# Kernel optimization log

Measured on AMD Instinct MI355X. Metric: run time of the kernel, lower is better.

The kernel has to match this reference:

```python
import jax, jax.numpy as jnp
import numpy as np

N, D, H, O, E = 50000, 512, 512, 256, 150000
NEG_SLOPE = 0.2
EPS = 1e-16


def gat_conv(x, edge_index, W_src, W_dst, a_src, a_dst, bias):
    """Single-head PyG GATConv, add_self_loops=False.
    x: [N, Din]; edge_index: [2, E] (row 0 = src, row 1 = dst).
    W_src/W_dst: [Din, C]; a_src/a_dst: [C]; bias: [C].
    """
    src, dst = edge_index[0], edge_index[1]
    h_src = x @ W_src                      # [N, C]
    h_dst = x @ W_dst                      # [N, C]
    alpha_src = h_src @ a_src              # [N]
    alpha_dst = h_dst @ a_dst              # [N]
    e = jax.nn.leaky_relu(alpha_src[src] + alpha_dst[dst], NEG_SLOPE)  # [E]
    # per-destination segment softmax (numerically stable)
    m = jax.ops.segment_max(e, dst, num_segments=N)       # [N]
    ex = jnp.exp(e - m[dst])                               # [E]
    s = jax.ops.segment_sum(ex, dst, num_segments=N)       # [N]
    alpha = ex / (s[dst] + EPS)                            # [E]
    # scatter-add weighted source messages to destinations
    out = jax.ops.segment_sum(alpha[:, None] * h_src[src], dst, num_segments=N)  # [N, C]
    return out + bias


def setup_inputs() -> dict:
    key = jax.random.key(0)
    ks = jax.random.split(key, 20)
    g = lambda i, shape, sc: (jax.random.normal(ks[i], shape, dtype=jnp.float32) * sc)
    inp = {
        "x": jax.random.normal(ks[0], (N, D), dtype=jnp.float32),
        "edge_index": jax.random.randint(ks[1], (2, E), 0, N, dtype=jnp.int32),
        "edge_index_2_hop": jax.random.randint(ks[2], (2, E), 0, N, dtype=jnp.int32),
        # conv1 (D -> H)
        "W1_src": g(3, (D, H), 0.05), "W1_dst": g(4, (D, H), 0.05),
        "a1_src": g(5, (H,), 0.05), "a1_dst": g(6, (H,), 0.05),
        "b1": jnp.zeros((H,), jnp.float32),
        # lin1 (H -> H)
        "Wl1": g(7, (H, H), 0.05), "bl1": jnp.zeros((H,), jnp.float32),
        # conv2 (H -> O)
        "W2_src": g(8, (H, O), 0.05), "W2_dst": g(9, (H, O), 0.05),
        "a2_src": g(10, (O,), 0.05), "a2_dst": g(11, (O,), 0.05),
        "b2": jnp.zeros((O,), jnp.float32),
        # lin2 (O -> O)
        "Wl2": g(12, (O, O), 0.05), "bl2": jnp.zeros((O,), jnp.float32),
    }
    return inp


def reference(x, edge_index, edge_index_2_hop,
              W1_src, W1_dst, a1_src, a1_dst, b1, Wl1, bl1,
              W2_src, W2_dst, a2_src, a2_dst, b2, Wl2, bl2):
    h = (gat_conv(x, edge_index, W1_src, W1_dst, a1_src, a1_dst, b1)
         + gat_conv(x, edge_index_2_hop, W1_src, W1_dst, a1_src, a1_dst, b1))
    h = jax.nn.relu(h @ Wl1 + bl1)
    h = (gat_conv(h, edge_index, W2_src, W2_dst, a2_src, a2_dst, b2)
         + gat_conv(h, edge_index_2_hop, W2_src, W2_dst, a2_src, a2_dst, b2))
    return h @ Wl2 + bl2
```

## Files before the change

kernel.cpp:

```cpp
#include <hip/hip_runtime.h>

typedef unsigned short u16;
typedef __attribute__((ext_vector_type(8))) unsigned short v8u16;
typedef __attribute__((ext_vector_type(4))) unsigned short v4u16;
typedef __attribute__((ext_vector_type(8))) __bf16 v8bf;
typedef __attribute__((ext_vector_type(4))) float v4f;

#define NN 50000
#define EE 150000
#define SCAN_CHUNK 512
#define NB_PER_SET 98

__device__ inline float b2f(u16 u) {
    union { unsigned int i; float f; } x; x.i = ((unsigned int)u) << 16; return x.f;
}
__device__ inline u16 f2b(float f) {
    union { float f; unsigned int i; } x; x.f = f;
    unsigned int r = x.i + 0x7FFFu + ((x.i >> 16) & 1u);
    return (u16)(r >> 16);
}
__device__ inline float wred(float v) {
    v += __shfl_down(v, 32, 64);
    v += __shfl_down(v, 16, 64);
    v += __shfl_down(v, 8, 64);
    v += __shfl_down(v, 4, 64);
    v += __shfl_down(v, 2, 64);
    v += __shfl_down(v, 1, 64);
    return v;
}
__device__ inline int wred_i(int v) {
    v += __shfl_down(v, 32, 64);
    v += __shfl_down(v, 16, 64);
    v += __shfl_down(v, 8, 64);
    v += __shfl_down(v, 4, 64);
    v += __shfl_down(v, 2, 64);
    v += __shfl_down(v, 1, 64);
    return v;
}

__device__ __forceinline__ void gll16(const u16* g, u16* l) {
    __builtin_amdgcn_global_load_lds(
        (const __attribute__((address_space(1))) void*)g,
        (__attribute__((address_space(3))) void*)l, 16, 0, 0);
}


__global__ void transpose4(const float* __restrict__ W0, u16* __restrict__ T0,
                           const float* __restrict__ W1, u16* __restrict__ T1,
                           const float* __restrict__ W2, u16* __restrict__ T2,
                           const float* __restrict__ W3, u16* __restrict__ T3) {
    int idx = blockIdx.x * blockDim.x + threadIdx.x;
    const float* W; u16* T; int N, K, base;
    if (idx < 262144)      { W = W0; T = T0; K = 512; N = 512; base = 0; }
    else if (idx < 524288) { W = W1; T = T1; K = 512; N = 512; base = 262144; }
    else if (idx < 655360) { W = W2; T = T2; K = 512; N = 256; base = 524288; }
    else if (idx < 720896) { W = W3; T = T3; K = 256; N = 256; base = 655360; }
    else return;
    int i = idx - base;
    int n = i % N, k = i / N;
    T[(size_t)n * K + k] = f2b(W[i]);
}

__global__ void wv4(const float* __restrict__ Wa, const float* __restrict__ Wb,
                    const float* __restrict__ Wc, const float* __restrict__ Wd,
                    const float* __restrict__ aa, const float* __restrict__ ab,
                    const float* __restrict__ ac, const float* __restrict__ ad,
                    float* __restrict__ vbuf) {
    int rw = (blockIdx.x * blockDim.x + threadIdx.x) >> 6;
    int lane = threadIdx.x & 63;
    if (rw >= 2048) return;
    int seg = rw >> 9, r = rw & 511;
    const float* W; const float* a; int C;
    if (seg == 0)      { W = Wa; a = aa; C = 512; }
    else if (seg == 1) { W = Wb; a = ab; C = 512; }
    else if (seg == 2) { W = Wc; a = ac; C = 256; }
    else               { W = Wd; a = ad; C = 256; }
    float s = 0.f;
    int c0 = lane * 8;
    if (c0 < C) {
        const float* wp = W + (size_t)r * C + c0;
        v4f w0 = *(const v4f*)wp;
        v4f w1 = *(const v4f*)(wp + 4);
        v4f a0 = *(const v4f*)(a + c0);
        v4f a1 = *(const v4f*)(a + c0 + 4);
#pragma unroll
        for (int j = 0; j < 4; ++j) s += w0[j] * a0[j] + w1[j] * a1[j];
    }
    s = wred(s);
    if (lane == 0) vbuf[rw] = s;
}

__global__ void alpha_pair_f32x(const float* __restrict__ X, const float* __restrict__ vs,
                                const float* __restrict__ vd, float* __restrict__ as_,
                                float* __restrict__ ad_, u16* __restrict__ Xb, int Nn) {
    int w = (blockIdx.x * blockDim.x + threadIdx.x) >> 6;
    int lane = threadIdx.x & 63;
    if (w >= Nn) return;
    const float* xp = X + (size_t)w * 512 + lane * 8;
    v4f x0 = *(const v4f*)xp;
    v4f x1 = *(const v4f*)(xp + 4);
    const float* vsp = vs + lane * 8;
    const float* vdp = vd + lane * 8;
    float s1 = 0.f, s2 = 0.f;
    v8u16 o;
#pragma unroll
    for (int j = 0; j < 4; ++j) {
        s1 += x0[j] * vsp[j] + x1[j] * vsp[j + 4];
        s2 += x0[j] * vdp[j] + x1[j] * vdp[j + 4];
        o[j] = f2b(x0[j]); o[j + 4] = f2b(x1[j]);
    }
    *(v8u16*)(Xb + (size_t)w * 512 + lane * 8) = o;
    s1 = wred(s1);
    s2 = wred(s2);
    if (lane == 0) { as_[w] = s1; ad_[w] = s2; }
}


__global__ void deg2_kernel(const int* __restrict__ ei1, const int* __restrict__ ei2,
                            int* __restrict__ deg) {
    int idx = blockIdx.x * blockDim.x + threadIdx.x;
    if (idx >= 2 * EE) return;
    int set = idx >= EE;
    int e = idx - set * EE;
    const int* ei = set ? ei2 : ei1;
    atomicAdd(&deg[set * NN + ei[EE + e]], 1);
}

__global__ void scan_partial(const int* __restrict__ deg, int* __restrict__ bsum) {
    int b = blockIdx.x;
    int set = b / NB_PER_SET, lb = b - set * NB_PER_SET;
    int tid = threadIdx.x;
    int i0 = lb * SCAN_CHUNK + tid * 2;
    int s = 0;
    if (i0 < NN)     s += deg[set * NN + i0];
    if (i0 + 1 < NN) s += deg[set * NN + i0 + 1];
    s = wred_i(s);
    __shared__ int lsum[4];
    if ((tid & 63) == 0) lsum[tid >> 6] = s;
    __syncthreads();
    if (tid == 0) bsum[b] = lsum[0] + lsum[1] + lsum[2] + lsum[3];
}

__global__ void scan_tops(int* __restrict__ bsum) {
    __shared__ int ls[256];
    int tid = threadIdx.x;
    int set = tid >> 7, lb = tid & 127;
    int v = (lb < NB_PER_SET) ? bsum[set * NB_PER_SET + lb] : 0;
    ls[tid] = v;
    __syncthreads();
    for (int off = 1; off < 128; off <<= 1) {
        int t = (lb >= off) ? ls[tid - off] : 0;
        __syncthreads();
        ls[tid] += t;
        __syncthreads();
    }
    if (lb < NB_PER_SET) bsum[set * NB_PER_SET + lb] = ls[tid] - v;
}

__global__ void scan_final(const int* __restrict__ deg, const int* __restrict__ bsum,
                           int* __restrict__ rp) {
    int b = blockIdx.x;
    int set = b / NB_PER_SET, lb = b - set * NB_PER_SET;
    int tid = threadIdx.x;
    int i0 = lb * SCAN_CHUNK + tid * 2;
    int d0 = (i0 < NN)     ? deg[set * NN + i0]     : 0;
    int d1 = (i0 + 1 < NN) ? deg[set * NN + i0 + 1] : 0;
    int pair = d0 + d1;
    __shared__ int ps[256];
    ps[tid] = pair;
    __syncthreads();
    for (int off = 1; off < 256; off <<= 1) {
        int t = (tid >= off) ? ps[tid - off] : 0;
        __syncthreads();
        ps[tid] += t;
        __syncthreads();
    }
    int base = bsum[b] + ps[tid] - pair;
    if (i0 < NN)     rp[set * (NN + 1) + i0] = base;
    if (i0 + 1 < NN) rp[set * (NN + 1) + i0 + 1] = base + d0;
    if (b == 0 && tid == 0) { rp[NN] = EE; rp[(NN + 1) + NN] = EE; }
}

__global__ void fill2_kernel(const int* __restrict__ ei1, const int* __restrict__ ei2,
                             const int* __restrict__ rp, int* __restrict__ deg,
                             int* __restrict__ srcp, int* __restrict__ dstp) {
    int idx = blockIdx.x * blockDim.x + threadIdx.x;
    if (idx >= 2 * EE) return;
    int set = idx >= EE;
    int e = idx - set * EE;
    const int* ei = set ? ei2 : ei1;
    int d = ei[EE + e];
    int old = atomicSub(&deg[set * NN + d], 1);
    int pos = rp[set * (NN + 1) + d] + old - 1;
    srcp[set * EE + pos] = ei[e];
    dstp[set * EE + pos] = d;
}

__global__ void edge_ex(const int* __restrict__ srcp, const int* __restrict__ dstp,
                        const float* __restrict__ asrc, const float* __restrict__ adst,
                        float* __restrict__ ex) {
    int i = blockIdx.x * blockDim.x + threadIdx.x;
    if (i >= 2 * EE) return;
    float t = asrc[srcp[i]] + adst[dstp[i]];
    t = t > 0.f ? t : 0.2f * t;
    ex[i] = __expf(fminf(t, 60.f));
}

template <int CV>
__global__ void gat_pull(const int* __restrict__ rp, const int* __restrict__ srcp,
                         const float* __restrict__ ex, const u16* __restrict__ H,
                         const float* __restrict__ bias, u16* __restrict__ G, int Nn) {
    const int C = CV * 64;
    int d = (blockIdx.x * blockDim.x + threadIdx.x) >> 6;
    int lane = threadIdx.x & 63;
    if (d >= Nn) return;
    float out[CV];
#pragma unroll
    for (int j = 0; j < CV; ++j) out[j] = 0.f;
#pragma unroll
    for (int set = 0; set < 2; ++set) {
        const int* rpS = rp + set * (NN + 1);
        int base = set * EE;
        int beg = rpS[d], end = rpS[d + 1];
        float acc[CV];
#pragma unroll
        for (int j = 0; j < CV; ++j) acc[j] = 0.f;
        float ssum = 0.f;
        for (int i = beg; i < end; ++i) {
            float w = ex[base + i];
            int s = srcp[base + i];
            ssum += w;
            const u16* hp = H + (size_t)s * C + lane * CV;
            if constexpr (CV == 8) {
                v8u16 hv = *(const v8u16*)hp;
#pragma unroll
                for (int j = 0; j < 8; ++j) acc[j] += w * b2f(hv[j]);
            } else {
                v4u16 hv = *(const v4u16*)hp;
#pragma unroll
                for (int j = 0; j < 4; ++j) acc[j] += w * b2f(hv[j]);
            }
        }
        float inv = 1.f / (ssum + 1e-16f);
#pragma unroll
        for (int j = 0; j < CV; ++j) out[j] += acc[j] * inv;
    }
    const float* bp = bias + lane * CV;
    u16* gp = G + (size_t)d * C + lane * CV;
    if constexpr (CV == 8) {
        v8u16 o;
#pragma unroll
        for (int j = 0; j < 8; ++j) o[j] = f2b(out[j] + 2.f * bp[j]);
        *(v8u16*)gp = o;
    } else {
        v4u16 o;
#pragma unroll
        for (int j = 0; j < 4; ++j) o[j] = f2b(out[j] + 2.f * bp[j]);
        *(v4u16*)gp = o;
    }
}

__global__ __launch_bounds__(256, 2) void gemm_bf16(
    const u16* __restrict__ A, const u16* __restrict__ Bt, void* __restrict__ Cv,
    int M, int N, int K, const float* __restrict__ bias, int relu, int outf32,
    const float* __restrict__ avs, const float* __restrict__ avd,
    float* __restrict__ aout_s, float* __restrict__ aout_d) {
    __shared__ u16 As[128 * 64];
    __shared__ u16 Bs[128 * 64];
    const int tid = threadIdx.x;
    const int lane = tid & 63;
    const int wid = tid >> 6;
    const int wm = wid >> 1;
    const int wn = wid & 1;
    const int quad = lane >> 4;
    const int l16 = lane & 15;

    const int nwg = gridDim.x * gridDim.y;
    const int orig = blockIdx.y * gridDim.x + blockIdx.x;
    const int q = nwg >> 3, r = nwg & 7;
    const int xcd = orig & 7, loc = orig >> 3;
    const int wg = (xcd < r ? xcd * (q + 1) : r * (q + 1) + (xcd - r) * q) + loc;
    const int tileM = (wg / gridDim.x) * 128;
    const int tileN = (wg % gridDim.x) * 128;

    const int srow = tid >> 3;
    const int scol = 8 * ((tid & 7) ^ ((tid >> 3) & 7));
    int ra0 = tileM + srow;       if (ra0 >= M) ra0 = M - 1;
    int ra1 = tileM + 32 + srow;  if (ra1 >= M) ra1 = M - 1;
    int ra2 = tileM + 64 + srow;  if (ra2 >= M) ra2 = M - 1;
    int ra3 = tileM + 96 + srow;  if (ra3 >= M) ra3 = M - 1;
    const u16* gA0 = A + (size_t)ra0 * K + scol;
    const u16* gA1 = A + (size_t)ra1 * K + scol;
    const u16* gA2 = A + (size_t)ra2 * K + scol;
    const u16* gA3 = A + (size_t)ra3 * K + scol;
    const u16* gB0 = Bt + (size_t)(tileN + srow) * K + scol;
    const u16* gB1 = Bt + (size_t)(tileN + 32 + srow) * K + scol;
    const u16* gB2 = Bt + (size_t)(tileN + 64 + srow) * K + scol;
    const u16* gB3 = Bt + (size_t)(tileN + 96 + srow) * K + scol;
    u16* lA0 = As + 0 * 2048 + wid * 512;
    u16* lA1 = As + 1 * 2048 + wid * 512;
    u16* lA2 = As + 2 * 2048 + wid * 512;
    u16* lA3 = As + 3 * 2048 + wid * 512;
    u16* lB0 = Bs + 0 * 2048 + wid * 512;
    u16* lB1 = Bs + 1 * 2048 + wid * 512;
    u16* lB2 = Bs + 2 * 2048 + wid * 512;
    u16* lB3 = Bs + 3 * 2048 + wid * 512;

    v4f acc[4][4];
#pragma unroll
    for (int i = 0; i < 4; ++i)
#pragma unroll
        for (int j = 0; j < 4; ++j) acc[i][j] = v4f{0.f, 0.f, 0.f, 0.f};

    for (int k0 = 0; k0 < K; k0 += 64) {
        gll16(gA0 + k0, lA0);
        gll16(gA1 + k0, lA1);
        gll16(gA2 + k0, lA2);
        gll16(gA3 + k0, lA3);
        gll16(gB0 + k0, lB0);
        gll16(gB1 + k0, lB1);
        gll16(gB2 + k0, lB2);
        gll16(gB3 + k0, lB3);
        __syncthreads();
#pragma unroll
        for (int ks = 0; ks < 2; ++ks) {
            const int cblk = ((((ks << 2) | quad) ^ (l16 & 7)) << 3);
            v8bf af[4], bfr[4];
#pragma unroll
            for (int i = 0; i < 4; ++i)
                af[i] = __builtin_bit_cast(v8bf,
                    *(const v8u16*)&As[(wm * 64 + i * 16 + l16) * 64 + cblk]);
#pragma unroll
            for (int i = 0; i < 4; ++i)
                bfr[i] = __builtin_bit_cast(v8bf,
                    *(const v8u16*)&Bs[(wn * 64 + i * 16 + l16) * 64 + cblk]);
#pragma unroll
            for (int mi = 0; mi < 4; ++mi)
#pragma unroll
                for (int ni = 0; ni < 4; ++ni)
                    acc[mi][ni] = __builtin_amdgcn_mfma_f32_16x16x32_bf16(af[mi], bfr[ni], acc[mi][ni], 0, 0, 0);
        }
        __syncthreads();
    }

    float rs[4][4], rd[4][4];
#pragma unroll
    for (int mi = 0; mi < 4; ++mi)
#pragma unroll
        for (int rr = 0; rr < 4; ++rr) { rs[mi][rr] = 0.f; rd[mi][rr] = 0.f; }

#pragma unroll
    for (int mi = 0; mi < 4; ++mi)
#pragma unroll
        for (int ni = 0; ni < 4; ++ni) {
            int col = tileN + wn * 64 + ni * 16 + l16;
            float bb = bias ? bias[col] : 0.f;
            float ws_ = avs ? avs[col] : 0.f;
            float wd_ = avd ? avd[col] : 0.f;
            int row0 = tileM + wm * 64 + mi * 16 + quad * 4;
#pragma unroll
            for (int rr = 0; rr < 4; ++rr) {
                int row = row0 + rr;
                if (row < M) {
                    float v = acc[mi][ni][rr] + bb;
                    if (relu) v = fmaxf(v, 0.f);
                    if (outf32) ((float*)Cv)[(size_t)row * N + col] = v;
                    else        ((u16*)Cv)[(size_t)row * N + col] = f2b(v);
                    rs[mi][rr] += v * ws_;
                    rd[mi][rr] += v * wd_;
                }
            }
        }

    if (avs) {
#pragma unroll
        for (int mi = 0; mi < 4; ++mi)
#pragma unroll
            for (int rr = 0; rr < 4; ++rr) {
                int row = tileM + wm * 64 + mi * 16 + quad * 4 + rr;
                float a = rs[mi][rr], b = rd[mi][rr];
                a += __shfl_down(a, 8, 64); a += __shfl_down(a, 4, 64);
                a += __shfl_down(a, 2, 64); a += __shfl_down(a, 1, 64);
                b += __shfl_down(b, 8, 64); b += __shfl_down(b, 4, 64);
                b += __shfl_down(b, 2, 64); b += __shfl_down(b, 1, 64);
                if (l16 == 0 && row < M) {
                    atomicAdd(&aout_s[row], a);
                    atomicAdd(&aout_d[row], b);
                }
            }
    }
}


extern "C" void kernel_launch(void* const* d_in, const int* in_sizes, int n_in,
                              void* d_out, int out_size, void* d_ws, size_t ws_size,
                              hipStream_t stream) {
    const float* x  = (const float*)d_in[0];
    const int* ei1  = (const int*)d_in[1];
    const int* ei2  = (const int*)d_in[2];
    const float* W1s = (const float*)d_in[3];
    const float* W1d = (const float*)d_in[4];
    const float* a1s = (const float*)d_in[5];
    const float* a1d = (const float*)d_in[6];
    const float* b1  = (const float*)d_in[7];
    const float* Wl1 = (const float*)d_in[8];
    const float* bl1 = (const float*)d_in[9];
    const float* W2s = (const float*)d_in[10];
    const float* W2d = (const float*)d_in[11];
    const float* a2s = (const float*)d_in[12];
    const float* a2d = (const float*)d_in[13];
    const float* b2  = (const float*)d_in[14];
    const float* Wl2 = (const float*)d_in[15];
    const float* bl2 = (const float*)d_in[16];
    float* out = (float*)d_out;

    char* ws = (char*)d_ws;
    size_t off = 0;
    auto alloc = [&](size_t b) { void* p = ws + off; off = (off + b + 255) & ~(size_t)255; return p; };
    u16* bufA   = (u16*)alloc((size_t)NN * 512 * 2);
    u16* bufB   = (u16*)alloc((size_t)NN * 512 * 2);
    int* rp     = (int*)alloc((size_t)2 * (NN + 1) * 4);
    int* srcp   = (int*)alloc((size_t)2 * EE * 4);
    int* dstp   = (int*)alloc((size_t)2 * EE * 4);
    int* deg    = (int*)alloc((size_t)2 * NN * 4);
    int* bsum   = (int*)alloc((size_t)2 * NB_PER_SET * 4);
    float* ex   = (float*)alloc((size_t)2 * EE * 4);
    float* asrc = (float*)alloc((size_t)NN * 4);
    float* adst = (float*)alloc((size_t)NN * 4);
    float* vbuf = (float*)alloc(2048 * 4);
    u16* Wt1s   = (u16*)alloc((size_t)512 * 512 * 2);
    u16* Wtl1   = (u16*)alloc((size_t)512 * 512 * 2);
    u16* Wt2s   = (u16*)alloc((size_t)512 * 256 * 2);
    u16* Wtl2   = (u16*)alloc((size_t)256 * 256 * 2);
    u16* g2buf  = bufB + (size_t)NN * 256;

    hipMemsetAsync(deg, 0, (size_t)2 * NN * 4, stream);
    deg2_kernel<<<(2 * EE + 255) / 256, 256, 0, stream>>>(ei1, ei2, deg);
    scan_partial<<<2 * NB_PER_SET, 256, 0, stream>>>(deg, bsum);
    scan_tops<<<1, 256, 0, stream>>>(bsum);
    scan_final<<<2 * NB_PER_SET, 256, 0, stream>>>(deg, bsum, rp);
    fill2_kernel<<<(2 * EE + 255) / 256, 256, 0, stream>>>(ei1, ei2, rp, deg, srcp, dstp);

    transpose4<<<(720896 + 255) / 256, 256, 0, stream>>>(W1s, Wt1s, Wl1, Wtl1, W2s, Wt2s, Wl2, Wtl2);
    wv4<<<512, 256, 0, stream>>>(W1s, W1d, W2s, W2d, a1s, a1d, a2s, a2d, vbuf);

    alpha_pair_f32x<<<(NN + 3) / 4, 256, 0, stream>>>(x, vbuf, vbuf + 512, asrc, adst, bufB, NN);
    edge_ex<<<(2 * EE + 255) / 256, 256, 0, stream>>>(srcp, dstp, asrc, adst, ex);
    gemm_bf16<<<dim3(4, 391), 256, 0, stream>>>(bufB, Wt1s, bufA, NN, 512, 512, nullptr, 0, 0,
                                                nullptr, nullptr, nullptr, nullptr);
    gat_pull<8><<<(NN + 3) / 4, 256, 0, stream>>>(rp, srcp, ex, bufA, b1, bufB, NN);
    hipMemsetAsync(asrc, 0, (size_t)NN * 4, stream);
    hipMemsetAsync(adst, 0, (size_t)NN * 4, stream);
    gemm_bf16<<<dim3(4, 391), 256, 0, stream>>>(bufB, Wtl1, bufA, NN, 512, 512, bl1, 1, 0,
                                                vbuf + 1024, vbuf + 1536, asrc, adst);

    edge_ex<<<(2 * EE + 255) / 256, 256, 0, stream>>>(srcp, dstp, asrc, adst, ex);
    gemm_bf16<<<dim3(2, 391), 256, 0, stream>>>(bufA, Wt2s, bufB, NN, 256, 512, nullptr, 0, 0,
                                                nullptr, nullptr, nullptr, nullptr);
    gat_pull<4><<<(NN + 3) / 4, 256, 0, stream>>>(rp, srcp, ex, bufB, b2, g2buf, NN);
    gemm_bf16<<<dim3(2, 391), 256, 0, stream>>>(g2buf, Wtl2, out, NN, 256, 256, bl2, 0, 1,
                                                nullptr, nullptr, nullptr, nullptr);

    (void)in_sizes; (void)n_in; (void)out_size; (void)ws_size;
}
```

Baseline: 517.7 us.

## Tile weight transpose, prefetch gather edges, fold memsets, drop XCD remap

The weight transpose now stages 32x32 tiles through shared memory so its global reads and writes are coalesced. The GAT pull loop keeps two edges in flight, so row loads overlap with the multiply-accumulate. Zeroing of the attention accumulators moves into the first pull kernel, replacing two memset launches. The GEMM tile mapping reverts to plain block indices and loses the XCD-aware swizzle, which may reduce L2 reuse across chiplets.

```diff
diff --git a/kernel.cpp b/kernel.cpp
--- a/kernel.cpp
+++ b/kernel.cpp
@@ -45,20 +45,33 @@
 }
 
 
-__global__ void transpose4(const float* __restrict__ W0, u16* __restrict__ T0,
-                           const float* __restrict__ W1, u16* __restrict__ T1,
-                           const float* __restrict__ W2, u16* __restrict__ T2,
-                           const float* __restrict__ W3, u16* __restrict__ T3) {
-    int idx = blockIdx.x * blockDim.x + threadIdx.x;
-    const float* W; u16* T; int N, K, base;
-    if (idx < 262144)      { W = W0; T = T0; K = 512; N = 512; base = 0; }
-    else if (idx < 524288) { W = W1; T = T1; K = 512; N = 512; base = 262144; }
-    else if (idx < 655360) { W = W2; T = T2; K = 512; N = 256; base = 524288; }
-    else if (idx < 720896) { W = W3; T = T3; K = 256; N = 256; base = 655360; }
-    else return;
-    int i = idx - base;
-    int n = i % N, k = i / N;
-    T[(size_t)n * K + k] = f2b(W[i]);
+__global__ void transpose4t(const float* __restrict__ W0, u16* __restrict__ T0,
+                            const float* __restrict__ W1, u16* __restrict__ T1,
+                            const float* __restrict__ W2, u16* __restrict__ T2,
+                            const float* __restrict__ W3, u16* __restrict__ T3) {
+    int b = blockIdx.x;
+    const float* W; u16* T; int N, K, t;
+    if (b < 256)      { W = W0; T = T0; K = 512; N = 512; t = b; }
+    else if (b < 512) { W = W1; T = T1; K = 512; N = 512; t = b - 256; }
+    else if (b < 640) { W = W2; T = T2; K = 512; N = 256; t = b - 512; }
+    else              { W = W3; T = T3; K = 256; N = 256; t = b - 640; }
+    const int tilesN = N >> 5;
+    const int kb = (t / tilesN) << 5;
+    const int nb = (t % tilesN) << 5;
+    __shared__ u16 tile[32][33];
+    const int c = threadIdx.x & 31;
+    const int r0 = threadIdx.x >> 5;
+#pragma unroll
+    for (int rr = 0; rr < 4; ++rr) {
+        int r = r0 + rr * 8;
+        tile[r][c] = f2b(W[(size_t)(kb + r) * N + nb + c]);
+    }
+    __syncthreads();
+#pragma unroll
+    for (int rr = 0; rr < 4; ++rr) {
+        int r = r0 + rr * 8;
+        T[(size_t)(nb + r) * K + kb + c] = tile[c][r];
+    }
 }
 
 __global__ void wv4(const float* __restrict__ Wa, const float* __restrict__ Wb,
@@ -209,9 +222,12 @@
 template <int CV>
 __global__ void gat_pull(const int* __restrict__ rp, const int* __restrict__ srcp,
                          const float* __restrict__ ex, const u16* __restrict__ H,
-                         const float* __restrict__ bias, u16* __restrict__ G, int Nn) {
+                         const float* __restrict__ bias, u16* __restrict__ G, int Nn,
+                         float* __restrict__ z1, float* __restrict__ z2) {
     const int C = CV * 64;
-    int d = (blockIdx.x * blockDim.x + threadIdx.x) >> 6;
+    int gid = blockIdx.x * blockDim.x + threadIdx.x;
+    if (z1 && gid < NN) { z1[gid] = 0.f; z2[gid] = 0.f; }
+    int d = gid >> 6;
     int lane = threadIdx.x & 63;
     if (d >= Nn) return;
     float out[CV];
@@ -226,19 +242,54 @@
 #pragma unroll
         for (int j = 0; j < CV; ++j) acc[j] = 0.f;
         float ssum = 0.f;
-        for (int i = beg; i < end; ++i) {
-            float w = ex[base + i];
-            int s = srcp[base + i];
-            ssum += w;
-            const u16* hp = H + (size_t)s * C + lane * CV;
+        int n = end - beg;
+        if (n > 0) {
+            const float* exS = ex + base;
+            const int* srcS = srcp + base;
             if constexpr (CV == 8) {
-                v8u16 hv = *(const v8u16*)hp;
-#pragma unroll
-                for (int j = 0; j < 8; ++j) acc[j] += w * b2f(hv[j]);
+                float w0 = exS[beg];
+                v8u16 h0 = *(const v8u16*)(H + (size_t)srcS[beg] * C + lane * 8);
+                float w1 = 0.f; v8u16 h1{};
+                if (n > 1) { w1 = exS[beg + 1]; h1 = *(const v8u16*)(H + (size_t)srcS[beg + 1] * C + lane * 8); }
+                for (int i = beg + 2; i < end; ++i) {
+                    float w2 = exS[i];
+                    v8u16 h2 = *(const v8u16*)(H + (size_t)srcS[i] * C + lane * 8);
+                    ssum += w0;
+#pragma unroll
+                    for (int j = 0; j < 8; ++j) acc[j] += w0 * b2f(h0[j]);
+                    w0 = w1; h0 = h1; w1 = w2; h1 = h2;
+                }
+                if (n > 1) {
+                    ssum += w0;
+#pragma unroll
+                    for (int j = 0; j < 8; ++j) acc[j] += w0 * b2f(h0[j]);
+                    w0 = w1; h0 = h1;
+                }
+                ssum += w0;
+#pragma unroll
+                for (int j = 0; j < 8; ++j) acc[j] += w0 * b2f(h0[j]);
             } else {
-                v4u16 hv = *(const v4u16*)hp;
-#pragma unroll
-                for (int j = 0; j < 4; ++j) acc[j] += w * b2f(hv[j]);
+                float w0 = exS[beg];
+                v4u16 h0 = *(const v4u16*)(H + (size_t)srcS[beg] * C + lane * 4);
+                float w1 = 0.f; v4u16 h1{};
+                if (n > 1) { w1 = exS[beg + 1]; h1 = *(const v4u16*)(H + (size_t)srcS[beg + 1] * C + lane * 4); }
+                for (int i = beg + 2; i < end; ++i) {
+                    float w2 = exS[i];
+                    v4u16 h2 = *(const v4u16*)(H + (size_t)srcS[i] * C + lane * 4);
+                    ssum += w0;
+#pragma unroll
+                    for (int j = 0; j < 4; ++j) acc[j] += w0 * b2f(h0[j]);
+                    w0 = w1; h0 = h1; w1 = w2; h1 = h2;
+                }
+                if (n > 1) {
+                    ssum += w0;
+#pragma unroll
+                    for (int j = 0; j < 4; ++j) acc[j] += w0 * b2f(h0[j]);
+                    w0 = w1; h0 = h1;
+                }
+                ssum += w0;
+#pragma unroll
+                for (int j = 0; j < 4; ++j) acc[j] += w0 * b2f(h0[j]);
             }
         }
         float inv = 1.f / (ssum + 1e-16f);
@@ -274,14 +325,8 @@
     const int wn = wid & 1;
     const int quad = lane >> 4;
     const int l16 = lane & 15;
-
-    const int nwg = gridDim.x * gridDim.y;
-    const int orig = blockIdx.y * gridDim.x + blockIdx.x;
-    const int q = nwg >> 3, r = nwg & 7;
-    const int xcd = orig & 7, loc = orig >> 3;
-    const int wg = (xcd < r ? xcd * (q + 1) : r * (q + 1) + (xcd - r) * q) + loc;
-    const int tileM = (wg / gridDim.x) * 128;
-    const int tileN = (wg % gridDim.x) * 128;
+    const int tileM = blockIdx.y * 128;
+    const int tileN = blockIdx.x * 128;
 
     const int srow = tid >> 3;
     const int scol = 8 * ((tid & 7) ^ ((tid >> 3) & 7));
@@ -441,23 +486,21 @@
     scan_final<<<2 * NB_PER_SET, 256, 0, stream>>>(deg, bsum, rp);
     fill2_kernel<<<(2 * EE + 255) / 256, 256, 0, stream>>>(ei1, ei2, rp, deg, srcp, dstp);
 
-    transpose4<<<(720896 + 255) / 256, 256, 0, stream>>>(W1s, Wt1s, Wl1, Wtl1, W2s, Wt2s, Wl2, Wtl2);
+    transpose4t<<<704, 256, 0, stream>>>(W1s, Wt1s, Wl1, Wtl1, W2s, Wt2s, Wl2, Wtl2);
     wv4<<<512, 256, 0, stream>>>(W1s, W1d, W2s, W2d, a1s, a1d, a2s, a2d, vbuf);
 
     alpha_pair_f32x<<<(NN + 3) / 4, 256, 0, stream>>>(x, vbuf, vbuf + 512, asrc, adst, bufB, NN);
     edge_ex<<<(2 * EE + 255) / 256, 256, 0, stream>>>(srcp, dstp, asrc, adst, ex);
     gemm_bf16<<<dim3(4, 391), 256, 0, stream>>>(bufB, Wt1s, bufA, NN, 512, 512, nullptr, 0, 0,
                                                 nullptr, nullptr, nullptr, nullptr);
-    gat_pull<8><<<(NN + 3) / 4, 256, 0, stream>>>(rp, srcp, ex, bufA, b1, bufB, NN);
-    hipMemsetAsync(asrc, 0, (size_t)NN * 4, stream);
-    hipMemsetAsync(adst, 0, (size_t)NN * 4, stream);
+    gat_pull<8><<<(NN + 3) / 4, 256, 0, stream>>>(rp, srcp, ex, bufA, b1, bufB, NN, asrc, adst);
     gemm_bf16<<<dim3(4, 391), 256, 0, stream>>>(bufB, Wtl1, bufA, NN, 512, 512, bl1, 1, 0,
                                                 vbuf + 1024, vbuf + 1536, asrc, adst);
 
     edge_ex<<<(2 * EE + 255) / 256, 256, 0, stream>>>(srcp, dstp, asrc, adst, ex);
     gemm_bf16<<<dim3(2, 391), 256, 0, stream>>>(bufA, Wt2s, bufB, NN, 256, 512, nullptr, 0, 0,
                                                 nullptr, nullptr, nullptr, nullptr);
-    gat_pull<4><<<(NN + 3) / 4, 256, 0, stream>>>(rp, srcp, ex, bufB, b2, g2buf, NN);
+    gat_pull<4><<<(NN + 3) / 4, 256, 0, stream>>>(rp, srcp, ex, bufB, b2, g2buf, NN, nullptr, nullptr);
     gemm_bf16<<<dim3(2, 391), 256, 0, stream>>>(g2buf, Wtl2, out, NN, 256, 256, bl2, 0, 1,
                                                 nullptr, nullptr, nullptr, nullptr);
 
```

Result: faster. 506.8 us (-2.1%).
